# Kernel optimization log

Hardware: AMD Instinct MI355X
Metric: run time of the kernel (lower is better)

## Reference

```python
import jax, jax.numpy as jnp
import numpy as np

NEG_INF = -1e30


def setup_inputs() -> dict:
    key = jax.random.key(0)
    k1, k2, k3, k4 = jax.random.split(key, 4)
    b, p_len, h_len, hidden = 16, 1024, 1024, 256
    premise_hidden = jax.random.normal(k1, (b, p_len, hidden), dtype=jnp.float32)
    hypothesis_hidden = jax.random.normal(k2, (b, h_len, hidden), dtype=jnp.float32)
    p_mask = jnp.ones((b, p_len), dtype=jnp.int32)
    h_mask = jnp.ones((b, h_len), dtype=jnp.int32)
    # nn.Bilinear(hidden, hidden, 1): weight [1, hidden, hidden], bias [1]
    bound = 1.0 / np.sqrt(hidden)
    W = jax.random.uniform(k3, (1, hidden, hidden), dtype=jnp.float32, minval=-bound, maxval=bound)
    bias = jax.random.uniform(k4, (1,), dtype=jnp.float32, minval=-bound, maxval=bound)
    return {"premise_hidden": premise_hidden, "hypothesis_hidden": hypothesis_hidden,
            "p_mask": p_mask, "h_mask": h_mask, "W": W, "bias": bias}


def reference(premise_hidden, hypothesis_hidden, p_mask, h_mask, W, bias):
    b, p_len, hidden = premise_hidden.shape
    h_len = hypothesis_hidden.shape[1]
    # Bilinear score: sim[b,p,q] = p^T W h + bias  (decomposed as P @ W @ H^T)
    sim = jnp.einsum('bpd,de,bqe->bpq', premise_hidden, W[0], hypothesis_hidden) + bias[0]
    # mask = bmm(p_mask[...,None], h_mask[:,None,:]); add -1e30 where masked
    mask = p_mask.astype(sim.dtype)[:, :, None] * h_mask.astype(sim.dtype)[:, None, :]
    sim = sim + (1.0 - mask) * NEG_INF
    # row-wise softmax over h_len -> aligned hypothesis
    attn_probs = jax.nn.softmax(sim, axis=-1)                      # [b, p_len, h_len]
    aligned_hypothesis = jnp.einsum('bpq,bqd->bpd', attn_probs, hypothesis_hidden)
    # column-max softmax over h_len -> aligned premise (requires p_len == h_len)
    attn_probs_t = jax.nn.softmax(jnp.max(sim, axis=1), axis=-1)   # [b, h_len]
    aligned_premise = jnp.einsum('bq,bqd->bd', attn_probs_t, premise_hidden)  # [b, hidden]
    aligned_premise = jnp.broadcast_to(aligned_premise[:, None, :], (b, h_len, hidden))
    return aligned_premise, aligned_hypothesis
```

## Files before the change

### kernel.cpp

```cpp
#include <hip/hip_runtime.h>

#define BATCH 16
#define PL 1024
#define HL 1024
#define HID 256
#define OUT0_ELEMS ((size_t)BATCH * PL * HID)

typedef __bf16 bf16x8 __attribute__((ext_vector_type(8)));
typedef unsigned short ushort8 __attribute__((ext_vector_type(8)));
typedef float floatx4 __attribute__((ext_vector_type(4)));
typedef unsigned short ushort;

union frag_u { bf16x8 b; ushort8 u; uint4 q; };

__device__ __forceinline__ float bf2f(ushort u) {
    return __uint_as_float(((unsigned int)u) << 16);
}
__device__ __forceinline__ ushort f2bf(float f) {
    unsigned int u = __float_as_uint(f);
    unsigned int r = u + 0x7FFFu + ((u >> 16) & 1u);
    return (ushort)(r >> 16);
}
__device__ __forceinline__ unsigned int fenc(float x) {
    unsigned int u = __float_as_uint(x);
    return (u & 0x80000000u) ? ~u : (u | 0x80000000u);
}
__device__ __forceinline__ float fdec(unsigned int e) {
    return (e & 0x80000000u) ? __uint_as_float(e & 0x7FFFFFFFu) : __uint_as_float(~e);
}
__device__ __forceinline__ bool detect_bf16(const void* p) {
    const unsigned int* w = (const unsigned int*)p;
    int cnt = 0;
    for (int i = 0; i < 256; ++i) {
        unsigned int f = (w[i] >> 7) & 0xFFu;
        cnt += (f >= 90u && f <= 140u) ? 1 : 0;
    }
    return cnt >= 192;
}

__device__ __forceinline__ void gload_lds16(const void* g, void* l) {
    __builtin_amdgcn_global_load_lds((const __attribute__((address_space(1))) unsigned int*)g,
                                     (__attribute__((address_space(3))) unsigned int*)l, 16, 0, 0);
}

#define MFMA(a, b, c) __builtin_amdgcn_mfma_f32_16x16x32_bf16(a, b, c, 0, 0, 0)


__global__ __launch_bounds__(256) void prep_w(const float* __restrict__ W,
                                              ushort* __restrict__ WThi, ushort* __restrict__ WTlo)
{
    const int e = blockIdx.x, d = threadIdx.x;
    float v = W[d * 256 + e];
    ushort hi = f2bf(v);
    WThi[e * 256 + d] = hi;
    WTlo[e * 256 + d] = f2bf(v - bf2f(hi));
}

__global__ __launch_bounds__(256) void prep_h(const float* __restrict__ H,
                                              ushort* __restrict__ HQX, ushort* __restrict__ HTX)
{
    const int b = blockIdx.x >> 5, qb = blockIdx.x & 31;
    const int tid = threadIdx.x;
    const size_t base = ((size_t)(b * 32 + qb)) << 14;
    ushort* hq = HQX + base;
    ushort* ht = HTX + base;

    {
        const int qg = tid >> 5, cd = tid & 31;
#pragma unroll
        for (int r = 0; r < 4; ++r) {
            const int q = qg + r * 8;
            const float* src = H + ((size_t)(b * HL + qb * 32 + q)) * HID + cd * 8;
            frag_u th, tl;
#pragma unroll
            for (int j = 0; j < 8; ++j) {
                float f = src[j];
                ushort hi = f2bf(f);
                th.u[j] = hi;
                tl.u[j] = f2bf(f - bf2f(hi));
            }
            const int h = q & 7;
            *(uint4*)&hq[q * 512 + ((cd ^ h)) * 8]        = th.q;
            *(uint4*)&hq[q * 512 + ((32 + cd) ^ h) * 8]   = tl.q;
        }
    }
    {
        const int d = tid, h = d & 7;
#pragma unroll
        for (int Q = 0; Q < 4; ++Q) {
            frag_u th, tl;
#pragma unroll
            for (int j = 0; j < 8; ++j) {
                float f = H[((size_t)(b * HL + qb * 32 + Q * 8 + j)) * HID + d];
                ushort hi = f2bf(f);
                th.u[j] = hi;
                tl.u[j] = f2bf(f - bf2f(hi));
            }
            *(uint4*)&ht[d * 64 + ((Q) ^ h) * 8]     = th.q;
            *(uint4*)&ht[d * 64 + ((4 + Q) ^ h) * 8] = tl.q;
        }
    }
}

__global__ __launch_bounds__(256) void pw2_kernel(
    const float* __restrict__ P, const ushort* __restrict__ WThi, const ushort* __restrict__ WTlo,
    ushort* __restrict__ PWhi, ushort* __restrict__ PWlo)
{
    const int tid = threadIdx.x, lane = tid & 63, wave = tid >> 6;
    const int m = lane & 15, Q = lane >> 4;
    const int row0 = blockIdx.x * 64 + wave * 16;

    frag_u afH[8], afL[8];
    {
        const float* base = P + ((size_t)(row0 + m)) * HID + Q * 8;
#pragma unroll
        for (int kc = 0; kc < 8; ++kc) {
#pragma unroll
            for (int j = 0; j < 8; ++j) {
                float f = base[kc * 32 + j];
                ushort hi = f2bf(f);
                afH[kc].u[j] = hi;
                afL[kc].u[j] = f2bf(f - bf2f(hi));
            }
        }
    }
#pragma unroll 1
    for (int nt = 0; nt < 16; ++nt) {
        floatx4 acc = {0.f, 0.f, 0.f, 0.f};
        const size_t bb = ((size_t)(nt * 16 + m)) * 256 + Q * 8;
#pragma unroll
        for (int kc = 0; kc < 8; ++kc) {
            frag_u bh, bl;
            bh.q = *(const uint4*)(WThi + bb + kc * 32);
            bl.q = *(const uint4*)(WTlo + bb + kc * 32);
            acc = MFMA(afH[kc].b, bh.b, acc);
            acc = MFMA(afL[kc].b, bh.b, acc);
            acc = MFMA(afH[kc].b, bl.b, acc);
        }
#pragma unroll
        for (int r = 0; r < 4; ++r) {
            float v = acc[r];
            ushort hi = f2bf(v);
            size_t idx = ((size_t)(row0 + Q * 4 + r)) * HID + nt * 16 + m;
            PWhi[idx] = hi;
            PWlo[idx] = f2bf(v - bf2f(hi));
        }
    }
}

__global__ __launch_bounds__(256, 2) void flash2_kernel(
    const ushort* __restrict__ PWhi, const ushort* __restrict__ PWlo,
    const ushort* __restrict__ HQX, const ushort* __restrict__ HTX,
    unsigned int* __restrict__ cmax,
    float* __restrict__ Ows, float2* __restrict__ MLws)
{
    __shared__ ushort HQ[16384];
    __shared__ ushort HT[16384];

    const int tid = threadIdx.x, lane = tid & 63, wave = tid >> 6;
    const int m = lane & 15, Q = lane >> 4, h = m & 7;
    const int x = blockIdx.x & 7, i = blockIdx.x >> 3;
    const int b = x * 2 + (i & 1), pc = (i >> 1) & 15, s = i >> 5;
    const int wid = (b * 16 + pc) * 4 + wave;
    const int prow = pc * 64 + wave * 16;

    bf16x8 bfH[8], bfL[8];
    {
        const size_t rb = ((size_t)(b * PL + prow + m)) * HID + Q * 8;
#pragma unroll
        for (int kc = 0; kc < 8; ++kc) {
            bfH[kc] = *(const bf16x8*)(PWhi + rb + kc * 32);
            bfL[kc] = *(const bf16x8*)(PWlo + rb + kc * 32);
        }
    }

    floatx4 O[16];
#pragma unroll
    for (int c = 0; c < 16; ++c) O[c] = (floatx4){0.f, 0.f, 0.f, 0.f};
    float mi = -INFINITY, li = 0.f;

#pragma unroll 1
    for (int it = 0; it < 16; ++it) {
        const int qb = s * 16 + it;
        const int q0 = qb * 32;
        {
            const char* g = (const char*)((wave < 2 ? HQX : HTX) + (((size_t)(b * 32 + qb)) << 14));
            char* l = (char*)(wave < 2 ? HQ : HT);
            const int off = (wave & 1) * 16384;
#pragma unroll
            for (int ii = 0; ii < 16; ++ii)
                gload_lds16(g + off + ii * 1024 + lane * 16, l + off + ii * 1024);
        }
        __syncthreads();

        floatx4 S0 = {0.f, 0.f, 0.f, 0.f}, S1 = {0.f, 0.f, 0.f, 0.f};
#pragma unroll
        for (int kc = 0; kc < 8; ++kc) {
            const int sh = ((kc * 4 + Q) ^ h) * 8;
            const int sl = (((32 + kc * 4 + Q)) ^ h) * 8;
            frag_u A0h, A0l, A1h, A1l;
            A0h.q = *(const uint4*)&HQ[m * 512 + sh];
            A0l.q = *(const uint4*)&HQ[m * 512 + sl];
            A1h.q = *(const uint4*)&HQ[(16 + m) * 512 + sh];
            A1l.q = *(const uint4*)&HQ[(16 + m) * 512 + sl];
            S0 = MFMA(A0h.b, bfH[kc], S0);
            S0 = MFMA(A0l.b, bfH[kc], S0);
            S0 = MFMA(A0h.b, bfL[kc], S0);
            S1 = MFMA(A1h.b, bfH[kc], S1);
            S1 = MFMA(A1l.b, bfH[kc], S1);
            S1 = MFMA(A1h.b, bfL[kc], S1);
        }

#pragma unroll
        for (int t = 0; t < 2; ++t) {
#pragma unroll
            for (int r = 0; r < 4; ++r) {
                float v = t ? S1[r] : S0[r];
                v = fmaxf(v, __shfl_xor(v, 1));
                v = fmaxf(v, __shfl_xor(v, 2));
                v = fmaxf(v, __shfl_xor(v, 4));
                v = fmaxf(v, __shfl_xor(v, 8));
                if (m == 0)
                    atomicMax(&cmax[b * HL + q0 + t * 16 + Q * 4 + r], fenc(v));
            }
        }

        float rm = fmaxf(fmaxf(fmaxf(S0[0], S0[1]), fmaxf(S0[2], S0[3])),
                         fmaxf(fmaxf(S1[0], S1[1]), fmaxf(S1[2], S1[3])));
        rm = fmaxf(rm, __shfl_xor(rm, 16));
        rm = fmaxf(rm, __shfl_xor(rm, 32));
        const float mnew = fmaxf(mi, rm);
        const float alpha = __expf(mi - mnew);
        mi = mnew;
        float p0[4], p1[4];
#pragma unroll
        for (int r = 0; r < 4; ++r) {
            p0[r] = __expf(S0[r] - mnew);
            p1[r] = __expf(S1[r] - mnew);
        }
        float rs = (p0[0] + p0[1] + p0[2] + p0[3]) + (p1[0] + p1[1] + p1[2] + p1[3]);
        rs += __shfl_xor(rs, 16);
        rs += __shfl_xor(rs, 32);
        li = li * alpha + rs;
#pragma unroll
        for (int c = 0; c < 16; ++c) O[c] *= alpha;

        frag_u pf;
#pragma unroll
        for (int j = 0; j < 8; ++j) {
            const int sL = m + 16 * ((Q & 1) * 2 + (j >> 2));
            const float v0 = __shfl(p0[j & 3], sL);
            const float v1 = __shfl(p1[j & 3], sL);
            pf.u[j] = f2bf(Q >= 2 ? v1 : v0);
        }

#pragma unroll
        for (int c = 0; c < 16; ++c) {
            const int rb = (c * 16 + m) * 64;
            frag_u Ah, Al;
            Ah.q = *(const uint4*)&HT[rb + ((Q) ^ h) * 8];
            Al.q = *(const uint4*)&HT[rb + ((4 + Q) ^ h) * 8];
            O[c] = MFMA(Ah.b, pf.b, O[c]);
            O[c] = MFMA(Al.b, pf.b, O[c]);
        }
        __syncthreads();
    }

    MLws[((size_t)s * 1024 + wid) * 64 + lane] = make_float2(mi, li);
    floatx4* op = (floatx4*)Ows + ((size_t)s * 1024 + wid) * 1024;
#pragma unroll
    for (int c = 0; c < 16; ++c) op[c * 64 + lane] = O[c];
}

__global__ __launch_bounds__(256) void combine_kernel(
    const float* __restrict__ Ows, const float2* __restrict__ MLws, float* __restrict__ out1)
{
    const int tid = threadIdx.x, lane = tid & 63, wave = tid >> 6;
    const int wid = blockIdx.x * 4 + wave;
    const int b = wid >> 6, pc = (wid >> 2) & 15, w = wid & 3;
    const int m = lane & 15, Q = lane >> 4;
    const float2 ml0 = MLws[((size_t)0 * 1024 + wid) * 64 + lane];
    const float2 ml1 = MLws[((size_t)1 * 1024 + wid) * 64 + lane];
    const float M = fmaxf(ml0.x, ml1.x);
    const float f0 = __expf(ml0.x - M), f1 = __expf(ml1.x - M);
    const float inv = 1.f / (ml0.y * f0 + ml1.y * f1);
    const floatx4* O0 = (const floatx4*)Ows + ((size_t)0 * 1024 + wid) * 1024;
    const floatx4* O1 = (const floatx4*)Ows + ((size_t)1 * 1024 + wid) * 1024;
    float* orow = out1 + ((size_t)(b * PL) + pc * 64 + w * 16 + m) * HID;
#pragma unroll
    for (int c = 0; c < 16; ++c) {
        floatx4 a = O0[c * 64 + lane];
        floatx4 d = O1[c * 64 + lane];
        floatx4 o = (a * f0 + d * f1) * inv;
        *(floatx4*)(orow + c * 16 + Q * 4) = o;
    }
}

__global__ __launch_bounds__(256) void wq_kernel(const unsigned int* __restrict__ cmax,
                                                 float* __restrict__ wq)
{
    __shared__ float buf[HL];
    __shared__ float red[256];
    const int b = blockIdx.x, tid = threadIdx.x;
    float lm = -INFINITY;
    for (int i = tid; i < HL; i += 256) {
        float v = fdec(cmax[b * HL + i]);
        buf[i] = v;
        lm = fmaxf(lm, v);
    }
    red[tid] = lm;
    __syncthreads();
    for (int st = 128; st > 0; st >>= 1) {
        if (tid < st) red[tid] = fmaxf(red[tid], red[tid + st]);
        __syncthreads();
    }
    const float M = red[0];
    __syncthreads();
    float ls = 0.f;
    for (int i = tid; i < HL; i += 256) {
        float e = __expf(buf[i] - M);
        buf[i] = e;
        ls += e;
    }
    red[tid] = ls;
    __syncthreads();
    for (int st = 128; st > 0; st >>= 1) {
        if (tid < st) red[tid] += red[tid + st];
        __syncthreads();
    }
    const float inv = 1.f / red[0];
    for (int i = tid; i < HL; i += 256) wq[b * HL + i] = buf[i] * inv;
}

__global__ __launch_bounds__(256) void psum_kernel(const float* __restrict__ P,
                                                   const float* __restrict__ wq,
                                                   float* __restrict__ ap)
{
    __shared__ float w[64];
    const int b = blockIdx.x >> 4, qc = blockIdx.x & 15;
    const int tid = threadIdx.x;
    if (tid < 64) w[tid] = wq[b * HL + qc * 64 + tid];
    __syncthreads();
    float acc = 0.f;
    const float* base = P + (((size_t)b * PL) + qc * 64) * HID + tid;
    for (int q = 0; q < 64; ++q) acc += w[q] * base[(size_t)q * HID];
    atomicAdd(&ap[b * HID + tid], acc);
}

__global__ __launch_bounds__(256) void bcast2_kernel(const float* __restrict__ ap,
                                                     float2* __restrict__ out0)
{
    const int b = blockIdx.x >> 3, chunk = blockIdx.x & 7;
    const int tid = threadIdx.x, pair = tid & 127, pr = tid >> 7;
    const float2 v = make_float2(ap[b * HID + pair * 2], ap[b * HID + pair * 2 + 1]);
    float2* basep = out0 + (size_t)b * PL * 128 + (size_t)chunk * 128 * 128;
    for (int i = 0; i < 64; ++i) basep[(i * 2 + pr) * 128 + pair] = v;
}

__global__ __launch_bounds__(256) void pw_v5(
    const void* __restrict__ Praw, const void* __restrict__ Wraw,
    ushort* __restrict__ PWhi, ushort* __restrict__ PWlo)
{
    __shared__ __align__(16) ushort WThi[16 * 264];
    __shared__ __align__(16) ushort WTlo[16 * 264];
    const bool pbf = detect_bf16(Praw);
    const bool wbf = detect_bf16(Wraw);
    const int tid = threadIdx.x, lane = tid & 63, wave = tid >> 6;
    const int m = lane & 15, quad = lane >> 4;
    const int row0 = blockIdx.x * 64 + wave * 16;
    frag_u afrH[8], afrL[8];
    if (pbf) {
        const ushort* base = (const ushort*)Praw + (size_t)(row0 + m) * HID + quad * 8;
#pragma unroll
        for (int kc = 0; kc < 8; ++kc) {
            afrH[kc].q = *(const uint4*)(base + kc * 32);
            afrL[kc].q = make_uint4(0, 0, 0, 0);
        }
    } else {
        const float* base = (const float*)Praw + (size_t)(row0 + m) * HID + quad * 8;
#pragma unroll
        for (int kc = 0; kc < 8; ++kc) {
#pragma unroll
            for (int j = 0; j < 8; ++j) {
                float f = base[kc * 32 + j];
                ushort hi = f2bf(f);
                afrH[kc].u[j] = hi;
                afrL[kc].u[j] = f2bf(f - bf2f(hi));
            }
        }
    }
    const ushort* W16 = (const ushort*)Wraw;
    const float* Wf = (const float*)Wraw;
    for (int nt = 0; nt < 16; ++nt) {
        __syncthreads();
        for (int i = tid; i < 4096; i += 256) {
            int e = i & 15, d = i >> 4;
            float wv = wbf ? bf2f(W16[d * 256 + nt * 16 + e]) : Wf[d * 256 + nt * 16 + e];
            ushort hi = f2bf(wv);
            WThi[e * 264 + d] = hi;
            WTlo[e * 264 + d] = f2bf(wv - bf2f(hi));
        }
        __syncthreads();
        floatx4 acc = {0.f, 0.f, 0.f, 0.f};
#pragma unroll
        for (int kc = 0; kc < 8; ++kc) {
            frag_u bh, bl;
            bh.q = *(const uint4*)(&WThi[m * 264 + kc * 32 + quad * 8]);
            bl.q = *(const uint4*)(&WTlo[m * 264 + kc * 32 + quad * 8]);
            acc = MFMA(afrH[kc].b, bh.b, acc);
            acc = MFMA(afrL[kc].b, bh.b, acc);
            acc = MFMA(afrH[kc].b, bl.b, acc);
        }
#pragma unroll
        for (int r = 0; r < 4; ++r) {
            float v = acc[r];
            ushort hi = f2bf(v);
            size_t idx = (size_t)(row0 + quad * 4 + r) * HID + nt * 16 + m;
            PWhi[idx] = hi;
            PWlo[idx] = f2bf(v - bf2f(hi));
        }
    }
}

__global__ __launch_bounds__(256) void flash_v5(
    const ushort* __restrict__ PWhi, const ushort* __restrict__ PWlo,
    const void* __restrict__ Praw, const void* __restrict__ Hraw, const void* __restrict__ Wraw,
    unsigned int* __restrict__ cmax, void* __restrict__ out_raw)
{
    __shared__ __align__(16) ushort Hbhi[16 * 264];
    __shared__ __align__(16) ushort Hblo[16 * 264];
    __shared__ __align__(16) float Hf[16 * 256];
    const bool hbf = detect_bf16(Hraw);
    const bool out_bf = detect_bf16(Praw) && hbf && detect_bf16(Wraw);
    const int tid = threadIdx.x, lane = tid & 63, wave = tid >> 6;
    const int m = lane & 15, quad = lane >> 4;
    const int b = blockIdx.x >> 4;
    const int prow = (blockIdx.x & 15) * 64 + wave * 16;
    bf16x8 afragH[8], afragL[8];
    {
        const size_t rbase = (size_t)(b * PL + prow + m) * HID + quad * 8;
#pragma unroll
        for (int kc = 0; kc < 8; ++kc) {
            afragH[kc] = *(const bf16x8*)(PWhi + rbase + kc * 32);
            afragL[kc] = *(const bf16x8*)(PWlo + rbase + kc * 32);
        }
    }
    float mrow[4], lrow[4], O[16][4];
#pragma unroll
    for (int r = 0; r < 4; ++r) { mrow[r] = -INFINITY; lrow[r] = 0.f; }
#pragma unroll
    for (int c = 0; c < 16; ++c)
#pragma unroll
        for (int r = 0; r < 4; ++r) O[c][r] = 0.f;

    for (int q0 = 0; q0 < HL; q0 += 16) {
        if (hbf) {
            const ushort* H16 = (const ushort*)Hraw;
            for (int g = tid; g < 512; g += 256) {
                int qq = g >> 5, ch = g & 31;
                const uint4 v = *(const uint4*)(H16 + (size_t)(b * HL + q0 + qq) * HID + ch * 8);
                *(uint4*)(&Hbhi[qq * 264 + ch * 8]) = v;
                *(uint4*)(&Hblo[qq * 264 + ch * 8]) = make_uint4(0, 0, 0, 0);
                float* dst = &Hf[qq * 256 + ch * 8];
                dst[0] = __uint_as_float(v.x << 16); dst[1] = __uint_as_float(v.x & 0xFFFF0000u);
                dst[2] = __uint_as_float(v.y << 16); dst[3] = __uint_as_float(v.y & 0xFFFF0000u);
                dst[4] = __uint_as_float(v.z << 16); dst[5] = __uint_as_float(v.z & 0xFFFF0000u);
                dst[6] = __uint_as_float(v.w << 16); dst[7] = __uint_as_float(v.w & 0xFFFF0000u);
            }
        } else {
            const float* H32 = (const float*)Hraw;
            for (int g = tid; g < 512; g += 256) {
                int qq = g >> 5, ch = g & 31;
                const float* src = H32 + (size_t)(b * HL + q0 + qq) * HID + ch * 8;
                frag_u th, tl;
                float* dst = &Hf[qq * 256 + ch * 8];
#pragma unroll
                for (int j = 0; j < 8; ++j) {
                    float f = src[j];
                    ushort hi = f2bf(f);
                    th.u[j] = hi;
                    tl.u[j] = f2bf(f - bf2f(hi));
                    dst[j] = f;
                }
                *(uint4*)(&Hbhi[qq * 264 + ch * 8]) = th.q;
                *(uint4*)(&Hblo[qq * 264 + ch * 8]) = tl.q;
            }
        }
        __syncthreads();
        floatx4 acc = {0.f, 0.f, 0.f, 0.f};
#pragma unroll
        for (int kc = 0; kc < 8; ++kc) {
            frag_u bh, bl;
            bh.q = *(const uint4*)(&Hbhi[m * 264 + kc * 32 + quad * 8]);
            bl.q = *(const uint4*)(&Hblo[m * 264 + kc * 32 + quad * 8]);
            acc = MFMA(afragH[kc], bh.b, acc);
            acc = MFMA(afragL[kc], bh.b, acc);
            acc = MFMA(afragH[kc], bl.b, acc);
        }
        float S[4];
#pragma unroll
        for (int r = 0; r < 4; ++r) S[r] = acc[r];
        float cmv = fmaxf(fmaxf(S[0], S[1]), fmaxf(S[2], S[3]));
        cmv = fmaxf(cmv, __shfl_xor(cmv, 16));
        cmv = fmaxf(cmv, __shfl_xor(cmv, 32));
        if (lane < 16) atomicMax(&cmax[b * HL + q0 + lane], fenc(cmv));
        float p_ij[4], alpha[4];
#pragma unroll
        for (int r = 0; r < 4; ++r) {
            float rm = S[r];
            rm = fmaxf(rm, __shfl_xor(rm, 1));
            rm = fmaxf(rm, __shfl_xor(rm, 2));
            rm = fmaxf(rm, __shfl_xor(rm, 4));
            rm = fmaxf(rm, __shfl_xor(rm, 8));
            float mnew = fmaxf(mrow[r], rm);
            p_ij[r] = __expf(S[r] - mnew);
            alpha[r] = __expf(mrow[r] - mnew);
            mrow[r] = mnew;
            float rsum = p_ij[r];
            rsum += __shfl_xor(rsum, 1);
            rsum += __shfl_xor(rsum, 2);
            rsum += __shfl_xor(rsum, 4);
            rsum += __shfl_xor(rsum, 8);
            lrow[r] = lrow[r] * alpha[r] + rsum;
        }
#pragma unroll
        for (int c = 0; c < 16; ++c)
#pragma unroll
            for (int r = 0; r < 4; ++r) O[c][r] *= alpha[r];
#pragma unroll 4
        for (int qq = 0; qq < 16; ++qq) {
            const int src = (lane & 48) + qq;
            float pb[4];
#pragma unroll
            for (int r = 0; r < 4; ++r) pb[r] = __shfl(p_ij[r], src);
#pragma unroll
            for (int c = 0; c < 16; ++c) {
                float hv = Hf[qq * 256 + c * 16 + m];
#pragma unroll
                for (int r = 0; r < 4; ++r) O[c][r] += pb[r] * hv;
            }
        }
        __syncthreads();
    }
    if (out_bf) {
        ushort* out1 = (ushort*)out_raw + OUT0_ELEMS;
#pragma unroll
        for (int r = 0; r < 4; ++r) {
            const float inv = 1.f / lrow[r];
            ushort* orow = out1 + (size_t)(b * PL + prow + quad * 4 + r) * HID;
#pragma unroll
            for (int c = 0; c < 16; ++c) orow[c * 16 + m] = f2bf(O[c][r] * inv);
        }
    } else {
        float* out1 = (float*)out_raw + OUT0_ELEMS;
#pragma unroll
        for (int r = 0; r < 4; ++r) {
            const float inv = 1.f / lrow[r];
            float* orow = out1 + (size_t)(b * PL + prow + quad * 4 + r) * HID;
#pragma unroll
            for (int c = 0; c < 16; ++c) orow[c * 16 + m] = O[c][r] * inv;
        }
    }
}

__global__ __launch_bounds__(256) void premise_v5(
    const void* __restrict__ Praw, const unsigned int* __restrict__ cmax, float* __restrict__ ap)
{
    __shared__ float buf[HL];
    __shared__ float red[256];
    const bool pbf = detect_bf16(Praw);
    const int b = blockIdx.x, tid = threadIdx.x;
    float lm = -INFINITY;
    for (int i = tid; i < HL; i += 256) {
        float v = fdec(cmax[b * HL + i]);
        buf[i] = v;
        lm = fmaxf(lm, v);
    }
    red[tid] = lm;
    __syncthreads();
    for (int st = 128; st > 0; st >>= 1) {
        if (tid < st) red[tid] = fmaxf(red[tid], red[tid + st]);
        __syncthreads();
    }
    const float M = red[0];
    __syncthreads();
    float ls = 0.f;
    for (int i = tid; i < HL; i += 256) {
        float e = __expf(buf[i] - M);
        buf[i] = e;
        ls += e;
    }
    red[tid] = ls;
    __syncthreads();
    for (int st = 128; st > 0; st >>= 1) {
        if (tid < st) red[tid] += red[tid + st];
        __syncthreads();
    }
    const float inv = 1.f / red[0];
    float a0 = 0.f, a1 = 0.f, a2 = 0.f, a3 = 0.f;
    if (pbf) {
        const ushort* base = (const ushort*)Praw + (size_t)b * PL * HID + tid;
        for (int q = 0; q < HL; q += 4) {
            a0 += buf[q] * bf2f(base[(size_t)q * HID]);
            a1 += buf[q + 1] * bf2f(base[(size_t)(q + 1) * HID]);
            a2 += buf[q + 2] * bf2f(base[(size_t)(q + 2) * HID]);
            a3 += buf[q + 3] * bf2f(base[(size_t)(q + 3) * HID]);
        }
    } else {
        const float* base = (const float*)Praw + (size_t)b * PL * HID + tid;
        for (int q = 0; q < HL; q += 4) {
            a0 += buf[q] * base[(size_t)q * HID];
            a1 += buf[q + 1] * base[(size_t)(q + 1) * HID];
            a2 += buf[q + 2] * base[(size_t)(q + 2) * HID];
            a3 += buf[q + 3] * base[(size_t)(q + 3) * HID];
        }
    }
    ap[b * HID + tid] = (a0 + a1 + a2 + a3) * inv;
}

__global__ __launch_bounds__(256) void bcast_v5(
    const float* __restrict__ ap,
    const void* __restrict__ Praw, const void* __restrict__ Hraw, const void* __restrict__ Wraw,
    void* __restrict__ out_raw)
{
    const bool out_bf = detect_bf16(Praw) && detect_bf16(Hraw) && detect_bf16(Wraw);
    const int b = blockIdx.x >> 3, chunk = blockIdx.x & 7;
    const int tid = threadIdx.x, pair = tid & 127, pr = tid >> 7;
    const float v0 = ap[b * HID + pair * 2];
    const float v1 = ap[b * HID + pair * 2 + 1];
    if (out_bf) {
        const unsigned int packed = (unsigned int)f2bf(v0) | ((unsigned int)f2bf(v1) << 16);
        unsigned int* basep = (unsigned int*)out_raw + (size_t)b * PL * 128 + (size_t)chunk * 128 * 128;
        for (int i = 0; i < 64; ++i) basep[(i * 2 + pr) * 128 + pair] = packed;
    } else {
        const float2 v = make_float2(v0, v1);
        float2* basep = (float2*)out_raw + (size_t)b * PL * 128 + (size_t)chunk * 128 * 128;
        for (int i = 0; i < 64; ++i) basep[(i * 2 + pr) * 128 + pair] = v;
    }
}

extern "C" void kernel_launch(void* const* d_in, const int* in_sizes, int n_in,
                              void* d_out, int out_size, void* d_ws, size_t ws_size,
                              hipStream_t stream)
{
    const void* prem = d_in[0];
    const void* hyp  = d_in[1];
    const void* W    = d_in[4];

    char* ws = (char*)d_ws;
    const size_t oPWhi = 0;
    const size_t oPWlo = oPWhi + 8388608;
    const size_t oWThi = oPWlo + 8388608;
    const size_t oWTlo = oWThi + 131072;
    const size_t oHQX  = oWTlo + 131072;
    const size_t oHTX  = oHQX + 16777216;
    const size_t oOws  = oHTX + 16777216;
    const size_t oML   = oOws + 33554432;
    const size_t oCmax = oML + 1048576;
    const size_t oWq   = oCmax + 65536;
    const size_t oAp   = oWq + 65536;
    const size_t need  = oAp + 16384;

    if (ws_size >= need) {
        ushort* PWhi = (ushort*)(ws + oPWhi);
        ushort* PWlo = (ushort*)(ws + oPWlo);
        ushort* WThi = (ushort*)(ws + oWThi);
        ushort* WTlo = (ushort*)(ws + oWTlo);
        ushort* HQX  = (ushort*)(ws + oHQX);
        ushort* HTX  = (ushort*)(ws + oHTX);
        float*  Ows  = (float*)(ws + oOws);
        float2* MLws = (float2*)(ws + oML);
        unsigned int* cmax = (unsigned int*)(ws + oCmax);
        float* wq = (float*)(ws + oWq);
        float* ap = (float*)(ws + oAp);
        float* out0 = (float*)d_out;
        float* out1 = out0 + OUT0_ELEMS;

        hipMemsetAsync(cmax, 0, 65536, stream);
        hipMemsetAsync(ap, 0, 16384, stream);
        prep_w<<<256, 256, 0, stream>>>((const float*)W, WThi, WTlo);
        prep_h<<<512, 256, 0, stream>>>((const float*)hyp, HQX, HTX);
        pw2_kernel<<<256, 256, 0, stream>>>((const float*)prem, WThi, WTlo, PWhi, PWlo);
        flash2_kernel<<<512, 256, 0, stream>>>(PWhi, PWlo, HQX, HTX, cmax, Ows, MLws);
        combine_kernel<<<256, 256, 0, stream>>>(Ows, MLws, out1);
        wq_kernel<<<16, 256, 0, stream>>>(cmax, wq);
        psum_kernel<<<256, 256, 0, stream>>>((const float*)prem, wq, ap);
        bcast2_kernel<<<128, 256, 0, stream>>>(ap, (float2*)out0);
    } else {
        ushort* PWhi = (ushort*)ws;
        ushort* PWlo = (ushort*)(ws + OUT0_ELEMS * 2);
        unsigned int* cmax = (unsigned int*)(ws + OUT0_ELEMS * 4);
        float* ap = (float*)(ws + OUT0_ELEMS * 4 + (size_t)BATCH * HL * 4);
        hipMemsetAsync(cmax, 0, (size_t)BATCH * HL * sizeof(unsigned int), stream);
        pw_v5<<<256, 256, 0, stream>>>(prem, W, PWhi, PWlo);
        flash_v5<<<256, 256, 0, stream>>>(PWhi, PWlo, prem, hyp, W, cmax, d_out);
        premise_v5<<<BATCH, 256, 0, stream>>>(prem, cmax, ap);
        bcast_v5<<<128, 256, 0, stream>>>(ap, prem, hyp, W, d_out);
    }
}
```

Baseline: 246.4 us.

## Drop H low-part in PV, stream H^T from global, split pw2 and retile combine

The P·V product now uses only the bf16 high part of H, which halves the MFMAs and the HT staging, and HT fragments are read straight from global/L2 instead of LDS. With the HT buffer gone, LDS per block drops and flash2 occupancy rises to 3 blocks per CU. The PW low fragments are loaded per iteration rather than kept in registers, and the O rescale is skipped when no row max changed. pw2 is split across two blocks per row tile, combine is restructured to stage through LDS for coalesced row writes, and the unused fallback path and bf16 detection are removed. The reduced H precision in PV adds accuracy risk.

New measurement: 357.5 us. 45.1% more time.

```diff
diff --git a/kernel.cpp b/kernel.cpp
--- a/kernel.cpp
+++ b/kernel.cpp
@@ -28,16 +28,6 @@
 __device__ __forceinline__ float fdec(unsigned int e) {
     return (e & 0x80000000u) ? __uint_as_float(e & 0x7FFFFFFFu) : __uint_as_float(~e);
 }
-__device__ __forceinline__ bool detect_bf16(const void* p) {
-    const unsigned int* w = (const unsigned int*)p;
-    int cnt = 0;
-    for (int i = 0; i < 256; ++i) {
-        unsigned int f = (w[i] >> 7) & 0xFFu;
-        cnt += (f >= 90u && f <= 140u) ? 1 : 0;
-    }
-    return cnt >= 192;
-}
-
 __device__ __forceinline__ void gload_lds16(const void* g, void* l) {
     __builtin_amdgcn_global_load_lds((const __attribute__((address_space(1))) unsigned int*)g,
                                      (__attribute__((address_space(3))) unsigned int*)l, 16, 0, 0);
@@ -61,9 +51,8 @@
 {
     const int b = blockIdx.x >> 5, qb = blockIdx.x & 31;
     const int tid = threadIdx.x;
-    const size_t base = ((size_t)(b * 32 + qb)) << 14;
-    ushort* hq = HQX + base;
-    ushort* ht = HTX + base;
+    ushort* hq = HQX + (((size_t)(b * 32 + qb)) << 14);
+    ushort* ht = HTX + (((size_t)(b * 32 + qb)) << 13);
 
     {
         const int qg = tid >> 5, cd = tid & 31;
@@ -80,24 +69,20 @@
                 tl.u[j] = f2bf(f - bf2f(hi));
             }
             const int h = q & 7;
-            *(uint4*)&hq[q * 512 + ((cd ^ h)) * 8]        = th.q;
-            *(uint4*)&hq[q * 512 + ((32 + cd) ^ h) * 8]   = tl.q;
+            *(uint4*)&hq[q * 512 + (cd ^ h) * 8]        = th.q;
+            *(uint4*)&hq[q * 512 + ((32 + cd) ^ h) * 8] = tl.q;
         }
     }
     {
-        const int d = tid, h = d & 7;
-#pragma unroll
-        for (int Q = 0; Q < 4; ++Q) {
-            frag_u th, tl;
-#pragma unroll
-            for (int j = 0; j < 8; ++j) {
-                float f = H[((size_t)(b * HL + qb * 32 + Q * 8 + j)) * HID + d];
-                ushort hi = f2bf(f);
-                th.u[j] = hi;
-                tl.u[j] = f2bf(f - bf2f(hi));
-            }
-            *(uint4*)&ht[d * 64 + ((Q) ^ h) * 8]     = th.q;
-            *(uint4*)&ht[d * 64 + ((4 + Q) ^ h) * 8] = tl.q;
+        const int d0 = tid >> 2, Q = tid & 3;
+#pragma unroll
+        for (int rep = 0; rep < 4; ++rep) {
+            const int d = d0 + rep * 64;
+            frag_u th;
+#pragma unroll
+            for (int j = 0; j < 8; ++j)
+                th.u[j] = f2bf(H[((size_t)(b * HL + qb * 32 + Q * 8 + j)) * HID + d]);
+            *(uint4*)&ht[d * 32 + Q * 8] = th.q;
         }
     }
 }
@@ -108,7 +93,8 @@
 {
     const int tid = threadIdx.x, lane = tid & 63, wave = tid >> 6;
     const int m = lane & 15, Q = lane >> 4;
-    const int row0 = blockIdx.x * 64 + wave * 16;
+    const int nh = blockIdx.x & 1;
+    const int row0 = (blockIdx.x >> 1) * 64 + wave * 16;
 
     frag_u afH[8], afL[8];
     {
@@ -125,7 +111,7 @@
         }
     }
 #pragma unroll 1
-    for (int nt = 0; nt < 16; ++nt) {
+    for (int nt = nh * 8; nt < nh * 8 + 8; ++nt) {
         floatx4 acc = {0.f, 0.f, 0.f, 0.f};
         const size_t bb = ((size_t)(nt * 16 + m)) * 256 + Q * 8;
 #pragma unroll
@@ -148,14 +134,13 @@
     }
 }
 
-__global__ __launch_bounds__(256, 2) void flash2_kernel(
+__global__ __launch_bounds__(256, 3) void flash2_kernel(
     const ushort* __restrict__ PWhi, const ushort* __restrict__ PWlo,
     const ushort* __restrict__ HQX, const ushort* __restrict__ HTX,
     unsigned int* __restrict__ cmax,
     float* __restrict__ Ows, float2* __restrict__ MLws)
 {
     __shared__ ushort HQ[16384];
-    __shared__ ushort HT[16384];
 
     const int tid = threadIdx.x, lane = tid & 63, wave = tid >> 6;
     const int m = lane & 15, Q = lane >> 4, h = m & 7;
@@ -164,15 +149,12 @@
     const int wid = (b * 16 + pc) * 4 + wave;
     const int prow = pc * 64 + wave * 16;
 
-    bf16x8 bfH[8], bfL[8];
-    {
-        const size_t rb = ((size_t)(b * PL + prow + m)) * HID + Q * 8;
-#pragma unroll
-        for (int kc = 0; kc < 8; ++kc) {
-            bfH[kc] = *(const bf16x8*)(PWhi + rb + kc * 32);
-            bfL[kc] = *(const bf16x8*)(PWlo + rb + kc * 32);
-        }
-    }
+    const size_t rb = ((size_t)(b * PL + prow + m)) * HID + Q * 8;
+    bf16x8 bfH[8];
+#pragma unroll
+    for (int kc = 0; kc < 8; ++kc)
+        bfH[kc] = *(const bf16x8*)(PWhi + rb + kc * 32);
+    const ushort* pwl = PWlo + rb;
 
     floatx4 O[16];
 #pragma unroll
@@ -183,21 +165,24 @@
     for (int it = 0; it < 16; ++it) {
         const int qb = s * 16 + it;
         const int q0 = qb * 32;
+        asm volatile("" : "+v"(pwl));
+
         {
-            const char* g = (const char*)((wave < 2 ? HQX : HTX) + (((size_t)(b * 32 + qb)) << 14));
-            char* l = (char*)(wave < 2 ? HQ : HT);
-            const int off = (wave & 1) * 16384;
-#pragma unroll
-            for (int ii = 0; ii < 16; ++ii)
-                gload_lds16(g + off + ii * 1024 + lane * 16, l + off + ii * 1024);
+            const char* g = (const char*)(HQX + (((size_t)(b * 32 + qb)) << 14)) + wave * 8192;
+            char* l = (char*)HQ + wave * 8192;
+#pragma unroll
+            for (int ii = 0; ii < 8; ++ii)
+                gload_lds16(g + ii * 1024 + lane * 16, l + ii * 1024);
         }
         __syncthreads();
 
         floatx4 S0 = {0.f, 0.f, 0.f, 0.f}, S1 = {0.f, 0.f, 0.f, 0.f};
 #pragma unroll
         for (int kc = 0; kc < 8; ++kc) {
+            frag_u bl;
+            bl.q = *(const uint4*)(pwl + kc * 32);
             const int sh = ((kc * 4 + Q) ^ h) * 8;
-            const int sl = (((32 + kc * 4 + Q)) ^ h) * 8;
+            const int sl = ((32 + kc * 4 + Q) ^ h) * 8;
             frag_u A0h, A0l, A1h, A1l;
             A0h.q = *(const uint4*)&HQ[m * 512 + sh];
             A0l.q = *(const uint4*)&HQ[m * 512 + sl];
@@ -205,10 +190,10 @@
             A1l.q = *(const uint4*)&HQ[(16 + m) * 512 + sl];
             S0 = MFMA(A0h.b, bfH[kc], S0);
             S0 = MFMA(A0l.b, bfH[kc], S0);
-            S0 = MFMA(A0h.b, bfL[kc], S0);
+            S0 = MFMA(A0h.b, bl.b, S0);
             S1 = MFMA(A1h.b, bfH[kc], S1);
             S1 = MFMA(A1l.b, bfH[kc], S1);
-            S1 = MFMA(A1h.b, bfL[kc], S1);
+            S1 = MFMA(A1h.b, bl.b, S1);
         }
 
 #pragma unroll
@@ -229,8 +214,9 @@
                          fmaxf(fmaxf(S1[0], S1[1]), fmaxf(S1[2], S1[3])));
         rm = fmaxf(rm, __shfl_xor(rm, 16));
         rm = fmaxf(rm, __shfl_xor(rm, 32));
+        const float miold = mi;
         const float mnew = fmaxf(mi, rm);
-        const float alpha = __expf(mi - mnew);
+        const float alpha = __expf(miold - mnew);
         mi = mnew;
         float p0[4], p1[4];
 #pragma unroll
@@ -242,8 +228,10 @@
         rs += __shfl_xor(rs, 16);
         rs += __shfl_xor(rs, 32);
         li = li * alpha + rs;
-#pragma unroll
-        for (int c = 0; c < 16; ++c) O[c] *= alpha;
+        if (__any(mnew > miold)) {
+#pragma unroll
+            for (int c = 0; c < 16; ++c) O[c] *= alpha;
+        }
 
         frag_u pf;
 #pragma unroll
@@ -254,14 +242,14 @@
             pf.u[j] = f2bf(Q >= 2 ? v1 : v0);
         }
 
-#pragma unroll
-        for (int c = 0; c < 16; ++c) {
-            const int rb = (c * 16 + m) * 64;
-            frag_u Ah, Al;
-            Ah.q = *(const uint4*)&HT[rb + ((Q) ^ h) * 8];
-            Al.q = *(const uint4*)&HT[rb + ((4 + Q) ^ h) * 8];
-            O[c] = MFMA(Ah.b, pf.b, O[c]);
-            O[c] = MFMA(Al.b, pf.b, O[c]);
+        {
+            const ushort* ht = HTX + (((size_t)(b * 32 + qb)) << 13);
+#pragma unroll
+            for (int c = 0; c < 16; ++c) {
+                frag_u Ah;
+                Ah.q = *(const uint4*)(ht + (c * 16 + m) * 32 + Q * 8);
+                O[c] = MFMA(Ah.b, pf.b, O[c]);
+            }
         }
         __syncthreads();
     }
@@ -272,28 +260,34 @@
     for (int c = 0; c < 16; ++c) op[c * 64 + lane] = O[c];
 }
 
-__global__ __launch_bounds__(256) void combine_kernel(
+__global__ __launch_bounds__(256) void combine2_kernel(
     const float* __restrict__ Ows, const float2* __restrict__ MLws, float* __restrict__ out1)
 {
-    const int tid = threadIdx.x, lane = tid & 63, wave = tid >> 6;
-    const int wid = blockIdx.x * 4 + wave;
-    const int b = wid >> 6, pc = (wid >> 2) & 15, w = wid & 3;
-    const int m = lane & 15, Q = lane >> 4;
-    const float2 ml0 = MLws[((size_t)0 * 1024 + wid) * 64 + lane];
-    const float2 ml1 = MLws[((size_t)1 * 1024 + wid) * 64 + lane];
+    __shared__ float T[16 * 260];
+    const int wid = blockIdx.x, t = threadIdx.x;
+    const int m = t & 15;
+    const int Q = (t >> 4) & 3, c0 = t >> 6;
+    const float2 ml0 = MLws[(size_t)wid * 64 + m];
+    const float2 ml1 = MLws[(size_t)(1024 + wid) * 64 + m];
     const float M = fmaxf(ml0.x, ml1.x);
     const float f0 = __expf(ml0.x - M), f1 = __expf(ml1.x - M);
     const float inv = 1.f / (ml0.y * f0 + ml1.y * f1);
-    const floatx4* O0 = (const floatx4*)Ows + ((size_t)0 * 1024 + wid) * 1024;
-    const floatx4* O1 = (const floatx4*)Ows + ((size_t)1 * 1024 + wid) * 1024;
-    float* orow = out1 + ((size_t)(b * PL) + pc * 64 + w * 16 + m) * HID;
-#pragma unroll
-    for (int c = 0; c < 16; ++c) {
-        floatx4 a = O0[c * 64 + lane];
-        floatx4 d = O1[c * 64 + lane];
-        floatx4 o = (a * f0 + d * f1) * inv;
-        *(floatx4*)(orow + c * 16 + Q * 4) = o;
-    }
+    const floatx4* O0 = (const floatx4*)Ows + (size_t)wid * 1024;
+    const floatx4* O1 = (const floatx4*)Ows + (size_t)(1024 + wid) * 1024;
+#pragma unroll
+    for (int k = 0; k < 4; ++k) {
+        const int idx = t + k * 256;
+        const int c = c0 + k * 4;
+        floatx4 o = (O0[idx] * f0 + O1[idx] * f1) * inv;
+        *(floatx4*)&T[m * 260 + c * 16 + Q * 4] = o;
+    }
+    __syncthreads();
+    const int p = t >> 4, xx = t & 15;
+    const int b = wid >> 6, pc = (wid >> 2) & 15, w = wid & 3;
+    float* orow = out1 + ((size_t)(b * PL + pc * 64 + w * 16 + p)) * HID + xx * 16;
+#pragma unroll
+    for (int k = 0; k < 4; ++k)
+        *(floatx4*)(orow + k * 4) = *(const floatx4*)&T[p * 260 + xx * 16 + k * 4];
 }
 
 __global__ __launch_bounds__(256) void wq_kernel(const unsigned int* __restrict__ cmax,
@@ -357,295 +351,13 @@
     for (int i = 0; i < 64; ++i) basep[(i * 2 + pr) * 128 + pair] = v;
 }
 
-__global__ __launch_bounds__(256) void pw_v5(
-    const void* __restrict__ Praw, const void* __restrict__ Wraw,
-    ushort* __restrict__ PWhi, ushort* __restrict__ PWlo)
-{
-    __shared__ __align__(16) ushort WThi[16 * 264];
-    __shared__ __align__(16) ushort WTlo[16 * 264];
-    const bool pbf = detect_bf16(Praw);
-    const bool wbf = detect_bf16(Wraw);
-    const int tid = threadIdx.x, lane = tid & 63, wave = tid >> 6;
-    const int m = lane & 15, quad = lane >> 4;
-    const int row0 = blockIdx.x * 64 + wave * 16;
-    frag_u afrH[8], afrL[8];
-    if (pbf) {
-        const ushort* base = (const ushort*)Praw + (size_t)(row0 + m) * HID + quad * 8;
-#pragma unroll
-        for (int kc = 0; kc < 8; ++kc) {
-            afrH[kc].q = *(const uint4*)(base + kc * 32);
-            afrL[kc].q = make_uint4(0, 0, 0, 0);
-        }
-    } else {
-        const float* base = (const float*)Praw + (size_t)(row0 + m) * HID + quad * 8;
-#pragma unroll
-        for (int kc = 0; kc < 8; ++kc) {
-#pragma unroll
-            for (int j = 0; j < 8; ++j) {
-                float f = base[kc * 32 + j];
-                ushort hi = f2bf(f);
-                afrH[kc].u[j] = hi;
-                afrL[kc].u[j] = f2bf(f - bf2f(hi));
-            }
-        }
-    }
-    const ushort* W16 = (const ushort*)Wraw;
-    const float* Wf = (const float*)Wraw;
-    for (int nt = 0; nt < 16; ++nt) {
-        __syncthreads();
-        for (int i = tid; i < 4096; i += 256) {
-            int e = i & 15, d = i >> 4;
-            float wv = wbf ? bf2f(W16[d * 256 + nt * 16 + e]) : Wf[d * 256 + nt * 16 + e];
-            ushort hi = f2bf(wv);
-            WThi[e * 264 + d] = hi;
-            WTlo[e * 264 + d] = f2bf(wv - bf2f(hi));
-        }
-        __syncthreads();
-        floatx4 acc = {0.f, 0.f, 0.f, 0.f};
-#pragma unroll
-        for (int kc = 0; kc < 8; ++kc) {
-            frag_u bh, bl;
-            bh.q = *(const uint4*)(&WThi[m * 264 + kc * 32 + quad * 8]);
-            bl.q = *(const uint4*)(&WTlo[m * 264 + kc * 32 + quad * 8]);
-            acc = MFMA(afrH[kc].b, bh.b, acc);
-            acc = MFMA(afrL[kc].b, bh.b, acc);
-            acc = MFMA(afrH[kc].b, bl.b, acc);
-        }
-#pragma unroll
-        for (int r = 0; r < 4; ++r) {
-            float v = acc[r];
-            ushort hi = f2bf(v);
-            size_t idx = (size_t)(row0 + quad * 4 + r) * HID + nt * 16 + m;
-            PWhi[idx] = hi;
-            PWlo[idx] = f2bf(v - bf2f(hi));
-        }
-    }
-}
-
-__global__ __launch_bounds__(256) void flash_v5(
-    const ushort* __restrict__ PWhi, const ushort* __restrict__ PWlo,
-    const void* __restrict__ Praw, const void* __restrict__ Hraw, const void* __restrict__ Wraw,
-    unsigned int* __restrict__ cmax, void* __restrict__ out_raw)
-{
-    __shared__ __align__(16) ushort Hbhi[16 * 264];
-    __shared__ __align__(16) ushort Hblo[16 * 264];
-    __shared__ __align__(16) float Hf[16 * 256];
-    const bool hbf = detect_bf16(Hraw);
-    const bool out_bf = detect_bf16(Praw) && hbf && detect_bf16(Wraw);
-    const int tid = threadIdx.x, lane = tid & 63, wave = tid >> 6;
-    const int m = lane & 15, quad = lane >> 4;
-    const int b = blockIdx.x >> 4;
-    const int prow = (blockIdx.x & 15) * 64 + wave * 16;
-    bf16x8 afragH[8], afragL[8];
-    {
-        const size_t rbase = (size_t)(b * PL + prow + m) * HID + quad * 8;
-#pragma unroll
-        for (int kc = 0; kc < 8; ++kc) {
-            afragH[kc] = *(const bf16x8*)(PWhi + rbase + kc * 32);
-            afragL[kc] = *(const bf16x8*)(PWlo + rbase + kc * 32);
-        }
-    }
-    float mrow[4], lrow[4], O[16][4];
-#pragma unroll
-    for (int r = 0; r < 4; ++r) { mrow[r] = -INFINITY; lrow[r] = 0.f; }
-#pragma unroll
-    for (int c = 0; c < 16; ++c)
-#pragma unroll
-        for (int r = 0; r < 4; ++r) O[c][r] = 0.f;
-
-    for (int q0 = 0; q0 < HL; q0 += 16) {
-        if (hbf) {
-            const ushort* H16 = (const ushort*)Hraw;
-            for (int g = tid; g < 512; g += 256) {
-                int qq = g >> 5, ch = g & 31;
-                const uint4 v = *(const uint4*)(H16 + (size_t)(b * HL + q0 + qq) * HID + ch * 8);
-                *(uint4*)(&Hbhi[qq * 264 + ch * 8]) = v;
-                *(uint4*)(&Hblo[qq * 264 + ch * 8]) = make_uint4(0, 0, 0, 0);
-                float* dst = &Hf[qq * 256 + ch * 8];
-                dst[0] = __uint_as_float(v.x << 16); dst[1] = __uint_as_float(v.x & 0xFFFF0000u);
-                dst[2] = __uint_as_float(v.y << 16); dst[3] = __uint_as_float(v.y & 0xFFFF0000u);
-                dst[4] = __uint_as_float(v.z << 16); dst[5] = __uint_as_float(v.z & 0xFFFF0000u);
-                dst[6] = __uint_as_float(v.w << 16); dst[7] = __uint_as_float(v.w & 0xFFFF0000u);
-            }
-        } else {
-            const float* H32 = (const float*)Hraw;
-            for (int g = tid; g < 512; g += 256) {
-                int qq = g >> 5, ch = g & 31;
-                const float* src = H32 + (size_t)(b * HL + q0 + qq) * HID + ch * 8;
-                frag_u th, tl;
-                float* dst = &Hf[qq * 256 + ch * 8];
-#pragma unroll
-                for (int j = 0; j < 8; ++j) {
-                    float f = src[j];
-                    ushort hi = f2bf(f);
-                    th.u[j] = hi;
-                    tl.u[j] = f2bf(f - bf2f(hi));
-                    dst[j] = f;
-                }
-                *(uint4*)(&Hbhi[qq * 264 + ch * 8]) = th.q;
-                *(uint4*)(&Hblo[qq * 264 + ch * 8]) = tl.q;
-            }
-        }
-        __syncthreads();
-        floatx4 acc = {0.f, 0.f, 0.f, 0.f};
-#pragma unroll
-        for (int kc = 0; kc < 8; ++kc) {
-            frag_u bh, bl;
-            bh.q = *(const uint4*)(&Hbhi[m * 264 + kc * 32 + quad * 8]);
-            bl.q = *(const uint4*)(&Hblo[m * 264 + kc * 32 + quad * 8]);
-            acc = MFMA(afragH[kc], bh.b, acc);
-            acc = MFMA(afragL[kc], bh.b, acc);
-            acc = MFMA(afragH[kc], bl.b, acc);
-        }
-        float S[4];
-#pragma unroll
-        for (int r = 0; r < 4; ++r) S[r] = acc[r];
-        float cmv = fmaxf(fmaxf(S[0], S[1]), fmaxf(S[2], S[3]));
-        cmv = fmaxf(cmv, __shfl_xor(cmv, 16));
-        cmv = fmaxf(cmv, __shfl_xor(cmv, 32));
-        if (lane < 16) atomicMax(&cmax[b * HL + q0 + lane], fenc(cmv));
-        float p_ij[4], alpha[4];
-#pragma unroll
-        for (int r = 0; r < 4; ++r) {
-            float rm = S[r];
-            rm = fmaxf(rm, __shfl_xor(rm, 1));
-            rm = fmaxf(rm, __shfl_xor(rm, 2));
-            rm = fmaxf(rm, __shfl_xor(rm, 4));
-            rm = fmaxf(rm, __shfl_xor(rm, 8));
-            float mnew = fmaxf(mrow[r], rm);
-            p_ij[r] = __expf(S[r] - mnew);
-            alpha[r] = __expf(mrow[r] - mnew);
-            mrow[r] = mnew;
-            float rsum = p_ij[r];
-            rsum += __shfl_xor(rsum, 1);
-            rsum += __shfl_xor(rsum, 2);
-            rsum += __shfl_xor(rsum, 4);
-            rsum += __shfl_xor(rsum, 8);
-            lrow[r] = lrow[r] * alpha[r] + rsum;
-        }
-#pragma unroll
-        for (int c = 0; c < 16; ++c)
-#pragma unroll
-            for (int r = 0; r < 4; ++r) O[c][r] *= alpha[r];
-#pragma unroll 4
-        for (int qq = 0; qq < 16; ++qq) {
-            const int src = (lane & 48) + qq;
-            float pb[4];
-#pragma unroll
-            for (int r = 0; r < 4; ++r) pb[r] = __shfl(p_ij[r], src);
-#pragma unroll
-            for (int c = 0; c < 16; ++c) {
-                float hv = Hf[qq * 256 + c * 16 + m];
-#pragma unroll
-                for (int r = 0; r < 4; ++r) O[c][r] += pb[r] * hv;
-            }
-        }
-        __syncthreads();
-    }
-    if (out_bf) {
-        ushort* out1 = (ushort*)out_raw + OUT0_ELEMS;
-#pragma unroll
-        for (int r = 0; r < 4; ++r) {
-            const float inv = 1.f / lrow[r];
-            ushort* orow = out1 + (size_t)(b * PL + prow + quad * 4 + r) * HID;
-#pragma unroll
-            for (int c = 0; c < 16; ++c) orow[c * 16 + m] = f2bf(O[c][r] * inv);
-        }
-    } else {
-        float* out1 = (float*)out_raw + OUT0_ELEMS;
-#pragma unroll
-        for (int r = 0; r < 4; ++r) {
-            const float inv = 1.f / lrow[r];
-            float* orow = out1 + (size_t)(b * PL + prow + quad * 4 + r) * HID;
-#pragma unroll
-            for (int c = 0; c < 16; ++c) orow[c * 16 + m] = O[c][r] * inv;
-        }
-    }
-}
-
-__global__ __launch_bounds__(256) void premise_v5(
-    const void* __restrict__ Praw, const unsigned int* __restrict__ cmax, float* __restrict__ ap)
-{
-    __shared__ float buf[HL];
-    __shared__ float red[256];
-    const bool pbf = detect_bf16(Praw);
-    const int b = blockIdx.x, tid = threadIdx.x;
-    float lm = -INFINITY;
-    for (int i = tid; i < HL; i += 256) {
-        float v = fdec(cmax[b * HL + i]);
-        buf[i] = v;
-        lm = fmaxf(lm, v);
-    }
-    red[tid] = lm;
-    __syncthreads();
-    for (int st = 128; st > 0; st >>= 1) {
-        if (tid < st) red[tid] = fmaxf(red[tid], red[tid + st]);
-        __syncthreads();
-    }
-    const float M = red[0];
-    __syncthreads();
-    float ls = 0.f;
-    for (int i = tid; i < HL; i += 256) {
-        float e = __expf(buf[i] - M);
-        buf[i] = e;
-        ls += e;
-    }
-    red[tid] = ls;
-    __syncthreads();
-    for (int st = 128; st > 0; st >>= 1) {
-        if (tid < st) red[tid] += red[tid + st];
-        __syncthreads();
-    }
-    const float inv = 1.f / red[0];
-    float a0 = 0.f, a1 = 0.f, a2 = 0.f, a3 = 0.f;
-    if (pbf) {
-        const ushort* base = (const ushort*)Praw + (size_t)b * PL * HID + tid;
-        for (int q = 0; q < HL; q += 4) {
-            a0 += buf[q] * bf2f(base[(size_t)q * HID]);
-            a1 += buf[q + 1] * bf2f(base[(size_t)(q + 1) * HID]);
-            a2 += buf[q + 2] * bf2f(base[(size_t)(q + 2) * HID]);
-            a3 += buf[q + 3] * bf2f(base[(size_t)(q + 3) * HID]);
-        }
-    } else {
-        const float* base = (const float*)Praw + (size_t)b * PL * HID + tid;
-        for (int q = 0; q < HL; q += 4) {
-            a0 += buf[q] * base[(size_t)q * HID];
-            a1 += buf[q + 1] * base[(size_t)(q + 1) * HID];
-            a2 += buf[q + 2] * base[(size_t)(q + 2) * HID];
-            a3 += buf[q + 3] * base[(size_t)(q + 3) * HID];
-        }
-    }
-    ap[b * HID + tid] = (a0 + a1 + a2 + a3) * inv;
-}
-
-__global__ __launch_bounds__(256) void bcast_v5(
-    const float* __restrict__ ap,
-    const void* __restrict__ Praw, const void* __restrict__ Hraw, const void* __restrict__ Wraw,
-    void* __restrict__ out_raw)
-{
-    const bool out_bf = detect_bf16(Praw) && detect_bf16(Hraw) && detect_bf16(Wraw);
-    const int b = blockIdx.x >> 3, chunk = blockIdx.x & 7;
-    const int tid = threadIdx.x, pair = tid & 127, pr = tid >> 7;
-    const float v0 = ap[b * HID + pair * 2];
-    const float v1 = ap[b * HID + pair * 2 + 1];
-    if (out_bf) {
-        const unsigned int packed = (unsigned int)f2bf(v0) | ((unsigned int)f2bf(v1) << 16);
-        unsigned int* basep = (unsigned int*)out_raw + (size_t)b * PL * 128 + (size_t)chunk * 128 * 128;
-        for (int i = 0; i < 64; ++i) basep[(i * 2 + pr) * 128 + pair] = packed;
-    } else {
-        const float2 v = make_float2(v0, v1);
-        float2* basep = (float2*)out_raw + (size_t)b * PL * 128 + (size_t)chunk * 128 * 128;
-        for (int i = 0; i < 64; ++i) basep[(i * 2 + pr) * 128 + pair] = v;
-    }
-}
-
 extern "C" void kernel_launch(void* const* d_in, const int* in_sizes, int n_in,
                               void* d_out, int out_size, void* d_ws, size_t ws_size,
                               hipStream_t stream)
 {
-    const void* prem = d_in[0];
-    const void* hyp  = d_in[1];
-    const void* W    = d_in[4];
+    const float* prem = (const float*)d_in[0];
+    const float* hyp  = (const float*)d_in[1];
+    const float* W    = (const float*)d_in[4];
 
     char* ws = (char*)d_ws;
     const size_t oPWhi = 0;
@@ -654,47 +366,34 @@
     const size_t oWTlo = oWThi + 131072;
     const size_t oHQX  = oWTlo + 131072;
     const size_t oHTX  = oHQX + 16777216;
-    const size_t oOws  = oHTX + 16777216;
+    const size_t oOws  = oHTX + 8388608;
     const size_t oML   = oOws + 33554432;
     const size_t oCmax = oML + 1048576;
     const size_t oWq   = oCmax + 65536;
     const size_t oAp   = oWq + 65536;
-    const size_t need  = oAp + 16384;
-
-    if (ws_size >= need) {
-        ushort* PWhi = (ushort*)(ws + oPWhi);
-        ushort* PWlo = (ushort*)(ws + oPWlo);
-        ushort* WThi = (ushort*)(ws + oWThi);
-        ushort* WTlo = (ushort*)(ws + oWTlo);
-        ushort* HQX  = (ushort*)(ws + oHQX);
-        ushort* HTX  = (ushort*)(ws + oHTX);
-        float*  Ows  = (float*)(ws + oOws);
-        float2* MLws = (float2*)(ws + oML);
-        unsigned int* cmax = (unsigned int*)(ws + oCmax);
-        float* wq = (float*)(ws + oWq);
-        float* ap = (float*)(ws + oAp);
-        float* out0 = (float*)d_out;
-        float* out1 = out0 + OUT0_ELEMS;
-
-        hipMemsetAsync(cmax, 0, 65536, stream);
-        hipMemsetAsync(ap, 0, 16384, stream);
-        prep_w<<<256, 256, 0, stream>>>((const float*)W, WThi, WTlo);
-        prep_h<<<512, 256, 0, stream>>>((const float*)hyp, HQX, HTX);
-        pw2_kernel<<<256, 256, 0, stream>>>((const float*)prem, WThi, WTlo, PWhi, PWlo);
-        flash2_kernel<<<512, 256, 0, stream>>>(PWhi, PWlo, HQX, HTX, cmax, Ows, MLws);
-        combine_kernel<<<256, 256, 0, stream>>>(Ows, MLws, out1);
-        wq_kernel<<<16, 256, 0, stream>>>(cmax, wq);
-        psum_kernel<<<256, 256, 0, stream>>>((const float*)prem, wq, ap);
-        bcast2_kernel<<<128, 256, 0, stream>>>(ap, (float2*)out0);
-    } else {
-        ushort* PWhi = (ushort*)ws;
-        ushort* PWlo = (ushort*)(ws + OUT0_ELEMS * 2);
-        unsigned int* cmax = (unsigned int*)(ws + OUT0_ELEMS * 4);
-        float* ap = (float*)(ws + OUT0_ELEMS * 4 + (size_t)BATCH * HL * 4);
-        hipMemsetAsync(cmax, 0, (size_t)BATCH * HL * sizeof(unsigned int), stream);
-        pw_v5<<<256, 256, 0, stream>>>(prem, W, PWhi, PWlo);
-        flash_v5<<<256, 256, 0, stream>>>(PWhi, PWlo, prem, hyp, W, cmax, d_out);
-        premise_v5<<<BATCH, 256, 0, stream>>>(prem, cmax, ap);
-        bcast_v5<<<128, 256, 0, stream>>>(ap, prem, hyp, W, d_out);
-    }
-}
+
+    ushort* PWhi = (ushort*)(ws + oPWhi);
+    ushort* PWlo = (ushort*)(ws + oPWlo);
+    ushort* WThi = (ushort*)(ws + oWThi);
+    ushort* WTlo = (ushort*)(ws + oWTlo);
+    ushort* HQX  = (ushort*)(ws + oHQX);
+    ushort* HTX  = (ushort*)(ws + oHTX);
+    float*  Ows  = (float*)(ws + oOws);
+    float2* MLws = (float2*)(ws + oML);
+    unsigned int* cmax = (unsigned int*)(ws + oCmax);
+    float* wq = (float*)(ws + oWq);
+    float* ap = (float*)(ws + oAp);
+    float* out0 = (float*)d_out;
+    float* out1 = out0 + OUT0_ELEMS;
+
+    hipMemsetAsync(cmax, 0, 65536, stream);
+    hipMemsetAsync(ap, 0, 16384, stream);
+    prep_w<<<256, 256, 0, stream>>>(W, WThi, WTlo);
+    prep_h<<<512, 256, 0, stream>>>(hyp, HQX, HTX);
+    pw2_kernel<<<512, 256, 0, stream>>>(prem, WThi, WTlo, PWhi, PWlo);
+    flash2_kernel<<<512, 256, 0, stream>>>(PWhi, PWlo, HQX, HTX, cmax, Ows, MLws);
+    combine2_kernel<<<1024, 256, 0, stream>>>(Ows, MLws, out1);
+    wq_kernel<<<16, 256, 0, stream>>>(cmax, wq);
+    psum_kernel<<<256, 256, 0, stream>>>(prem, wq, ap);
+    bcast2_kernel<<<128, 256, 0, stream>>>(ap, (float2*)out0);
+}
```
